# Kernel tuning notes

Measured on AMD Instinct MI355X. Metric: run time of the kernel, lower is better.

The kernel has to match this reference:

```python
import jax, jax.numpy as jnp
import numpy as np

N_EDGE_TYPES = 5  # e_feat compared against 0..4 in message_func


def setup_inputs() -> dict:
    key = jax.random.key(0)
    k1, k2, k3, k4, k5 = jax.random.split(key, 5)
    N, D, E = 50000, 128, 800000
    graph_embedding = jax.random.normal(k1, (N, D), dtype=jnp.float32)
    # xavier_uniform for a (1, D) tensor: bound = sqrt(6 / (1 + D))
    bound = float(np.sqrt(6.0 / (1 + D)))
    weight = jax.random.uniform(k2, (1, D), dtype=jnp.float32, minval=-bound, maxval=bound)
    e_feat = jax.random.randint(k3, (E,), 0, N_EDGE_TYPES, dtype=jnp.int64)
    src = jax.random.randint(k4, (E,), 0, N, dtype=jnp.int64)
    dst = jax.random.randint(k5, (E,), 0, N, dtype=jnp.int64)
    return {"graph_embedding": graph_embedding, "weight": weight,
            "e_feat": e_feat, "src": src, "dst": dst}


def reference(graph_embedding, weight, e_feat, src, dst):
    N = graph_embedding.shape[0]
    # emb == ft == ft0 == ... == ft4 in the original module
    emb = jax.nn.elu(graph_embedding * weight)           # [N, D]
    sft = emb[src]                                       # [E, D] gather src features
    # message = ft_src + sum_t where(e == t, ft_src, 0)
    # since ft0..ft4 all alias emb, the masked sum collapses to
    # sft * (1 + [e in {0..4}]) with exactly one mask firing per edge type.
    et = e_feat.reshape(-1, 1).astype(jnp.float32)       # mirrors e_feat.reshape(-1,1).float()
    hit = (et == jnp.arange(N_EDGE_TYPES, dtype=jnp.float32)[None, :]).sum(axis=1)  # [E]
    msg = sft * (1.0 + hit)[:, None]                     # [E, D]
    # scatter-reduce (sum) over destination nodes == dgl fn.sum('m','ft')
    res = jax.ops.segment_sum(msg, dst, num_segments=N)  # [N, D]
    return res
```

## Files before the change

kernel.cpp:

```cpp
#include <hip/hip_runtime.h>
#include <hip/hip_fp16.h>
#include <math.h>

#define DFEAT 128
#define RSH 6
#define RSZ 64
#define NT  512
#define EPB 4096
#define EPQ (EPB / NT)
#define CHUNK 2048
#define MAXNR 1024
#define TILESH 9
#define TILE (1 << TILESH)
typedef unsigned long long u64;
typedef unsigned int u32;
typedef unsigned short u16;
#define ENDK 0xFFFFFFFFFFFFFFFFULL

__device__ __forceinline__ void elu_store(const float* x, const float* w,
                                          __half* emb2, int i) {
    float4 xv = ((const float4*)x)[i];
    float4 wv = ((const float4*)w)[i & (DFEAT / 4 - 1)];
    float a, r0, r1, r2, r3;
    a = xv.x * wv.x; r0 = 2.0f * (a > 0.0f ? a : (__expf(a) - 1.0f));
    a = xv.y * wv.y; r1 = 2.0f * (a > 0.0f ? a : (__expf(a) - 1.0f));
    a = xv.z * wv.z; r2 = 2.0f * (a > 0.0f ? a : (__expf(a) - 1.0f));
    a = xv.w * wv.w; r3 = 2.0f * (a > 0.0f ? a : (__expf(a) - 1.0f));
    __half2 h01 = __floats2half2_rn(r0, r1);
    __half2 h23 = __floats2half2_rn(r2, r3);
    uint2 pk;
    pk.x = *(u32*)&h01;
    pk.y = *(u32*)&h23;
    ((uint2*)emb2)[i] = pk;
}

__device__ __forceinline__ void scan_tsum_lds(const u32* tsum, u32* ts, int nT) {
    int tid = threadIdx.x;
    u32 v = (tid < nT) ? tsum[tid] : 0u;
    ts[tid] = v;
    __syncthreads();
    for (int d = 1; d < NT; d <<= 1) {
        u32 o = (tid >= d) ? ts[tid - d] : 0u;
        __syncthreads();
        ts[tid] += o;
        __syncthreads();
    }
    u32 incl = ts[tid];
    __syncthreads();
    ts[tid] = incl - v;
    __syncthreads();
}

__global__ __launch_bounds__(NT) void hist_elu_kernel(
        const float* __restrict__ x, const float* __restrict__ w,
        __half* __restrict__ emb2, int total4,
        const int* __restrict__ dst, int E,
        u32* __restrict__ ghist, int EB, int NR) {
    if ((int)blockIdx.x < EB) {
        __shared__ u32 hist[MAXNR];
        int tid = threadIdx.x;
        for (int i = tid; i < NR; i += NT) hist[i] = 0;
        __syncthreads();
        int base = blockIdx.x * EPB;
        for (int q = 0; q < EPQ; ++q) {
            int e = base + tid + q * NT;
            if (e < E) atomicAdd(&hist[(((u32)dst[e]) >> RSH) & (MAXNR - 1)], 1u);
        }
        __syncthreads();
        for (int r = tid; r < NR; r += NT)
            ghist[(size_t)r * EB + blockIdx.x] = hist[r];
    } else {
        int idx = (blockIdx.x - EB) * NT + threadIdx.x;
        if (idx < total4) elu_store(x, w, emb2, idx);
    }
}

__global__ __launch_bounds__(NT) void scan_tile_kernel(
        u32* __restrict__ g, u32* __restrict__ tsum, int M) {
    __shared__ u32 sc[NT];
    int tid = threadIdx.x;
    int i = (blockIdx.x << TILESH) + tid;
    u32 v = (i < M) ? g[i] : 0u;
    sc[tid] = v;
    __syncthreads();
    for (int d = 1; d < NT; d <<= 1) {
        u32 o = (tid >= d) ? sc[tid - d] : 0u;
        __syncthreads();
        sc[tid] += o;
        __syncthreads();
    }
    if (i < M) g[i] = sc[tid] - v;
    if (tid == NT - 1) tsum[blockIdx.x] = sc[NT - 1];
}

__global__ __launch_bounds__(NT) void scatter_pairs_kernel(
        const int* __restrict__ src, const int* __restrict__ dst, int E,
        const u32* __restrict__ ghist, const u32* __restrict__ tsum,
        int EB, int NR, int nT, u32* __restrict__ pairs) {
    __shared__ u32 ts[NT];
    __shared__ u32 off[MAXNR];
    int tid = threadIdx.x;
    scan_tsum_lds(tsum, ts, nT);
    for (int r = tid; r < NR; r += NT) {
        u32 idx = (u32)r * EB + blockIdx.x;
        off[r] = ghist[idx] + ts[idx >> TILESH];
    }
    __syncthreads();
    int base = blockIdx.x * EPB;
    for (int q = 0; q < EPQ; ++q) {
        int e = base + tid + q * NT;
        if (e < E) {
            u32 d = (u32)dst[e];
            u32 s = (u32)src[e];
            u32 p = atomicAdd(&off[(d >> RSH) & (MAXNR - 1)], 1u);
            if (p < (u32)E) pairs[p] = ((d & (RSZ - 1)) << 16) | s;
        }
    }
}

__global__ __launch_bounds__(NT) void gather_sort_kernel(
        const __half* __restrict__ emb2, const u32* __restrict__ pairs,
        const u32* __restrict__ ghist, const u32* __restrict__ tsum,
        int EB, int NR, int nT, int E,
        float* __restrict__ out, int N) {
    __shared__ u32 ts[NT];
    __shared__ u16 sorted[CHUNK];
    __shared__ u32 bcnt[RSZ + 1];
    __shared__ u32 bstart[RSZ + 1];
    int tid = threadIdx.x;
    scan_tsum_lds(tsum, ts, nT);
    int r = blockIdx.x;
    u32 ia = (u32)r * (u32)EB;
    u32 s0 = ghist[ia] + ts[ia >> TILESH];
    u32 s1 = (r + 1 < NR) ? (ghist[ia + EB] + ts[(ia + EB) >> TILESH]) : (u32)E;
    if (s0 > (u32)E) s0 = (u32)E;
    if (s1 > (u32)E) s1 = (u32)E;
    if (s1 < s0) s1 = s0;
    __syncthreads();
    const int wv = tid >> 6;
    const int lane = tid & 63;
    u32 pos = s0;
    do {
        int csz = 0;
        if (s1 > pos) {
            u32 rem = s1 - pos;
            csz = rem < (u32)CHUNK ? (int)rem : CHUNK;
        }
        if (tid < RSZ + 1) bcnt[tid] = 0;
        __syncthreads();
        u32 p0 = 0, p1 = 0, p2 = 0, p3 = 0;
        int  r0 = -1, r1 = -1, r2 = -1, r3 = -1;
        {
            int e0 = tid, e1 = tid + NT, e2 = tid + 2 * NT, e3 = tid + 3 * NT;
            if (e0 < csz) { p0 = pairs[pos + e0]; r0 = (int)(p0 >> 16); }
            if (e1 < csz) { p1 = pairs[pos + e1]; r1 = (int)(p1 >> 16); }
            if (e2 < csz) { p2 = pairs[pos + e2]; r2 = (int)(p2 >> 16); }
            if (e3 < csz) { p3 = pairs[pos + e3]; r3 = (int)(p3 >> 16); }
            if (r0 >= 0) atomicAdd(&bcnt[r0 & (RSZ - 1)], 1u);
            if (r1 >= 0) atomicAdd(&bcnt[r1 & (RSZ - 1)], 1u);
            if (r2 >= 0) atomicAdd(&bcnt[r2 & (RSZ - 1)], 1u);
            if (r3 >= 0) atomicAdd(&bcnt[r3 & (RSZ - 1)], 1u);
        }
        __syncthreads();
        if (tid < RSZ) {
            u32 vv = bcnt[tid];
            u32 inc = vv;
            for (int d = 1; d < RSZ; d <<= 1) {
                u32 o = __shfl_up(inc, d);
                if (lane >= d) inc += o;
            }
            bstart[tid] = inc - vv;
            bcnt[tid]   = inc - vv;
            if (tid == RSZ - 1) bstart[RSZ] = inc;
        }
        __syncthreads();
        if (r0 >= 0) { u32 p = atomicAdd(&bcnt[r0 & (RSZ - 1)], 1u); sorted[p & (CHUNK - 1)] = (u16)(p0 & 0xFFFFu); }
        if (r1 >= 0) { u32 p = atomicAdd(&bcnt[r1 & (RSZ - 1)], 1u); sorted[p & (CHUNK - 1)] = (u16)(p1 & 0xFFFFu); }
        if (r2 >= 0) { u32 p = atomicAdd(&bcnt[r2 & (RSZ - 1)], 1u); sorted[p & (CHUNK - 1)] = (u16)(p2 & 0xFFFFu); }
        if (r3 >= 0) { u32 p = atomicAdd(&bcnt[r3 & (RSZ - 1)], 1u); sorted[p & (CHUNK - 1)] = (u16)(p3 & 0xFFFFu); }
        __syncthreads();
        for (int rr = 0; rr < 8; ++rr) {
            int row = (wv << 3) + rr;
            int n = (r << RSH) + row;
            int jb = (int)bstart[row], je = (int)bstart[row + 1];
            float ax, ay;
            if (pos != s0 && n < N) {
                float2 t = ((const float2*)out)[(size_t)n * (DFEAT / 2) + lane];
                ax = t.x; ay = t.y;
            } else {
                ax = 0.0f; ay = 0.0f;
            }
            for (int j = jb; j < je; j += 8) {
                int last = je - 1;
                int j1 = j + 1 < last ? j + 1 : last;
                int j2 = j + 2 < last ? j + 2 : last;
                int j3 = j + 3 < last ? j + 3 : last;
                int j4 = j + 4 < last ? j + 4 : last;
                int j5 = j + 5 < last ? j + 5 : last;
                int j6 = j + 6 < last ? j + 6 : last;
                int j7 = j + 7 < last ? j + 7 : last;
                u32 q0 = (u32)sorted[j];
                u32 q1 = (u32)sorted[j1];
                u32 q2 = (u32)sorted[j2];
                u32 q3 = (u32)sorted[j3];
                u32 q4 = (u32)sorted[j4];
                u32 q5 = (u32)sorted[j5];
                u32 q6 = (u32)sorted[j6];
                u32 q7 = (u32)sorted[j7];
                u32 h0 = ((const u32*)(emb2 + (size_t)q0 * DFEAT))[lane];
                u32 h1 = ((const u32*)(emb2 + (size_t)q1 * DFEAT))[lane];
                u32 h2 = ((const u32*)(emb2 + (size_t)q2 * DFEAT))[lane];
                u32 h3 = ((const u32*)(emb2 + (size_t)q3 * DFEAT))[lane];
                u32 h4 = ((const u32*)(emb2 + (size_t)q4 * DFEAT))[lane];
                u32 h5 = ((const u32*)(emb2 + (size_t)q5 * DFEAT))[lane];
                u32 h6 = ((const u32*)(emb2 + (size_t)q6 * DFEAT))[lane];
                u32 h7 = ((const u32*)(emb2 + (size_t)q7 * DFEAT))[lane];
                float2 f0 = __half22float2(*(__half2*)&h0);
                ax += f0.x; ay += f0.y;
                if (j + 1 < je) { float2 f = __half22float2(*(__half2*)&h1); ax += f.x; ay += f.y; }
                if (j + 2 < je) { float2 f = __half22float2(*(__half2*)&h2); ax += f.x; ay += f.y; }
                if (j + 3 < je) { float2 f = __half22float2(*(__half2*)&h3); ax += f.x; ay += f.y; }
                if (j + 4 < je) { float2 f = __half22float2(*(__half2*)&h4); ax += f.x; ay += f.y; }
                if (j + 5 < je) { float2 f = __half22float2(*(__half2*)&h5); ax += f.x; ay += f.y; }
                if (j + 6 < je) { float2 f = __half22float2(*(__half2*)&h6); ax += f.x; ay += f.y; }
                if (j + 7 < je) { float2 f = __half22float2(*(__half2*)&h7); ax += f.x; ay += f.y; }
            }
            if (n < N)
                ((float2*)out)[(size_t)n * (DFEAT / 2) + lane] = make_float2(ax, ay);
        }
        __syncthreads();
        pos += CHUNK;
    } while (pos < s1);
}


__global__ void bin_elu_ll_kernel(const float* __restrict__ x,
                                  const float* __restrict__ w,
                                  __half* __restrict__ emb2, int total4,
                                  const int* __restrict__ src,
                                  const int* __restrict__ dst, int E,
                                  u64* __restrict__ head,
                                  u64* __restrict__ nxt,
                                  int binBlocks) {
    if ((int)blockIdx.x < binBlocks) {
        int base = blockIdx.x * 1024 + threadIdx.x;
        for (int q = 0; q < 4; ++q) {
            int e = base + q * 256;
            if (e < E) {
                int s = src[e];
                int d = dst[e];
                u64 old = atomicExch(&head[d], ((u64)(u32)s << 32) | (u32)e);
                nxt[e] = old;
            }
        }
    } else {
        int idx = (blockIdx.x - binBlocks) * blockDim.x + threadIdx.x;
        if (idx >= total4) return;
        elu_store(x, w, emb2, idx);
    }
}

__global__ void gather_ll_kernel(const __half* __restrict__ emb2,
                                 const u64* __restrict__ head,
                                 const u64* __restrict__ nxt,
                                 float* __restrict__ out, int N) {
    int wid = (blockIdx.x * blockDim.x + threadIdx.x) >> 6;
    int lane = threadIdx.x & 63;
    int nA = wid * 2;
    int nB = nA + 1;
    if (nA >= N) return;
    bool hasB = (nB < N);
    u64 curA = head[nA];
    u64 curB = hasB ? head[nB] : ENDK;
    float2 accA = make_float2(0.0f, 0.0f);
    float2 accB = make_float2(0.0f, 0.0f);
    while (curA != ENDK || curB != ENDK) {
        bool aA = (curA != ENDK);
        bool aB = (curB != ENDK);
        u64 cA = curA, cB = curB;
        u32 uA = 0, uB = 0;
        if (aA) uA = ((const u32*)(emb2 + ((size_t)(cA >> 32)) * DFEAT))[lane];
        if (aB) uB = ((const u32*)(emb2 + ((size_t)(cB >> 32)) * DFEAT))[lane];
        if (aA) curA = nxt[(u32)cA];
        if (aB) curB = nxt[(u32)cB];
        if (aA) {
            float2 f = __half22float2(*(__half2*)&uA);
            accA.x += f.x; accA.y += f.y;
        }
        if (aB) {
            float2 f = __half22float2(*(__half2*)&uB);
            accB.x += f.x; accB.y += f.y;
        }
    }
    ((float2*)(out + (size_t)nA * DFEAT))[lane] = accA;
    if (hasB) ((float2*)(out + (size_t)nB * DFEAT))[lane] = accB;
}

__global__ void scatter_fused_kernel(const float* __restrict__ x,
                                     const float* __restrict__ w,
                                     const int* __restrict__ src,
                                     const int* __restrict__ dst,
                                     float* __restrict__ out, int E) {
    int t = blockIdx.x * blockDim.x + threadIdx.x;
    int edge = t >> 5;
    int lane = t & 31;
    if (edge >= E) return;
    int s = src[edge];
    int d = dst[edge];
    float4 xv = ((const float4*)(x + (size_t)s * DFEAT))[lane];
    float4 wv = ((const float4*)w)[lane];
    float4 v;
    float a;
    a = xv.x * wv.x; v.x = 2.0f * (a > 0.0f ? a : (__expf(a) - 1.0f));
    a = xv.y * wv.y; v.y = 2.0f * (a > 0.0f ? a : (__expf(a) - 1.0f));
    a = xv.z * wv.z; v.z = 2.0f * (a > 0.0f ? a : (__expf(a) - 1.0f));
    a = xv.w * wv.w; v.w = 2.0f * (a > 0.0f ? a : (__expf(a) - 1.0f));
    float* op = out + (size_t)d * DFEAT + lane * 4;
    unsafeAtomicAdd(op + 0, v.x);
    unsafeAtomicAdd(op + 1, v.y);
    unsafeAtomicAdd(op + 2, v.z);
    unsafeAtomicAdd(op + 3, v.w);
}

extern "C" void kernel_launch(void* const* d_in, const int* in_sizes, int n_in,
                              void* d_out, int out_size, void* d_ws, size_t ws_size,
                              hipStream_t stream) {
    const float* x   = (const float*)d_in[0];
    const float* w   = (const float*)d_in[1];
    const int*   src = (const int*)d_in[3];
    const int*   dst = (const int*)d_in[4];
    float* out = (float*)d_out;

    const int ND = in_sizes[0];
    const int N  = ND / DFEAT;
    const int E  = in_sizes[2];

    const int EB = (E + EPB - 1) / EPB;
    const int NR = (N + RSZ - 1) >> RSH;
    const int M  = NR * EB;
    const int nT = (M + TILE - 1) >> TILESH;

    size_t emb_bytes   = ((size_t)ND * sizeof(__half) + 15) & ~(size_t)15;
    size_t ghist_bytes = ((size_t)M * sizeof(u32) + 15) & ~(size_t)15;
    size_t tsum_bytes  = ((size_t)NT * sizeof(u32) + 15) & ~(size_t)15;
    size_t pairs_bytes = ((size_t)E * sizeof(u32) + 15) & ~(size_t)15;
    size_t total_new = emb_bytes + ghist_bytes + tsum_bytes + pairs_bytes;

    size_t head64_bytes = ((size_t)N * sizeof(u64) + 15) & ~(size_t)15;
    size_t nxt64_bytes  = ((size_t)E * sizeof(u64) + 15) & ~(size_t)15;
    size_t total_old = emb_bytes + head64_bytes + nxt64_bytes;

    int total4 = ND / 4;

    if (ws_size >= total_new && N <= 65536 && NR <= MAXNR && nT <= NT) {
        char* p = (char*)d_ws;
        __half* emb2  = (__half*)p;  p += emb_bytes;
        u32*    ghist = (u32*)p;     p += ghist_bytes;
        u32*    tsum  = (u32*)p;     p += tsum_bytes;
        u32*    pairs = (u32*)p;

        int eluBlocks = (total4 + NT - 1) / NT;
        hist_elu_kernel<<<EB + eluBlocks, NT, 0, stream>>>(
            x, w, emb2, total4, dst, E, ghist, EB, NR);

        scan_tile_kernel<<<nT, NT, 0, stream>>>(ghist, tsum, M);

        scatter_pairs_kernel<<<EB, NT, 0, stream>>>(
            src, dst, E, ghist, tsum, EB, NR, nT, pairs);

        gather_sort_kernel<<<NR, NT, 0, stream>>>(
            emb2, pairs, ghist, tsum, EB, NR, nT, E, out, N);
    } else if (ws_size >= total_old) {
        char* p = (char*)d_ws;
        __half* emb2 = (__half*)p;  p += emb_bytes;
        u64*    head = (u64*)p;     p += head64_bytes;
        u64*    nxt  = (u64*)p;

        hipMemsetAsync(head, 0xFF, (size_t)N * sizeof(u64), stream);

        int eluBlocks256 = (total4 + 255) / 256;
        int binBlocks = (E + 1023) / 1024;
        bin_elu_ll_kernel<<<binBlocks + eluBlocks256, 256, 0, stream>>>(
            x, w, emb2, total4, src, dst, E, head, nxt, binBlocks);

        long long waves = (N + 1) / 2;
        long long thr = waves * 64;
        gather_ll_kernel<<<(int)((thr + 255) / 256), 256, 0, stream>>>(
            emb2, head, nxt, out, N);
    } else {
        hipMemsetAsync(d_out, 0, (size_t)out_size * sizeof(float), stream);
        long long threads = (long long)E * 32;
        scatter_fused_kernel<<<(int)((threads + 255) / 256), 256, 0, stream>>>(x, w, src, dst, out, E);
    }
}
```

Before: 138.9 us.

## Replace global scan with per-block local offsets and segment collection in gather

The global exclusive scan over the block-by-bucket histogram and its separate scan kernel are removed. Each edge block now computes local bucket offsets itself and writes its pairs contiguously within its own 8192-edge region, staged through LDS so the global writes are coalesced. The gather kernel scans per-block segment counts itself and copies each bucket's segments from all edge blocks into an LDS buffer before the local sort. This saves one launch and the global scan, at the cost of serial per-thread segment copies and a larger LDS footprint in the gather.

```diff
diff --git a/kernel.cpp b/kernel.cpp
--- a/kernel.cpp
+++ b/kernel.cpp
@@ -6,12 +6,10 @@
 #define RSH 6
 #define RSZ 64
 #define NT  512
-#define EPB 4096
+#define EPB 8192
 #define EPQ (EPB / NT)
-#define CHUNK 2048
+#define BUF 8192
 #define MAXNR 1024
-#define TILESH 9
-#define TILE (1 << TILESH)
 typedef unsigned long long u64;
 typedef unsigned int u32;
 typedef unsigned short u16;
@@ -34,157 +32,147 @@
     ((uint2*)emb2)[i] = pk;
 }
 
-__device__ __forceinline__ void scan_tsum_lds(const u32* tsum, u32* ts, int nT) {
-    int tid = threadIdx.x;
-    u32 v = (tid < nT) ? tsum[tid] : 0u;
-    ts[tid] = v;
-    __syncthreads();
-    for (int d = 1; d < NT; d <<= 1) {
-        u32 o = (tid >= d) ? ts[tid - d] : 0u;
-        __syncthreads();
-        ts[tid] += o;
-        __syncthreads();
-    }
-    u32 incl = ts[tid];
-    __syncthreads();
-    ts[tid] = incl - v;
-    __syncthreads();
-}
-
 __global__ __launch_bounds__(NT) void hist_elu_kernel(
         const float* __restrict__ x, const float* __restrict__ w,
         __half* __restrict__ emb2, int total4,
         const int* __restrict__ dst, int E,
-        u32* __restrict__ ghist, int EB, int NR) {
+        u32* __restrict__ loff, int EB, int NR) {
     if ((int)blockIdx.x < EB) {
-        __shared__ u32 hist[MAXNR];
+        __shared__ u32 cnt[MAXNR];
+        __shared__ u32 sb[NT];
         int tid = threadIdx.x;
-        for (int i = tid; i < NR; i += NT) hist[i] = 0;
+        for (int i = tid; i < NR; i += NT) cnt[i] = 0;
         __syncthreads();
         int base = blockIdx.x * EPB;
         for (int q = 0; q < EPQ; ++q) {
             int e = base + tid + q * NT;
-            if (e < E) atomicAdd(&hist[(((u32)dst[e]) >> RSH) & (MAXNR - 1)], 1u);
-        }
-        __syncthreads();
-        for (int r = tid; r < NR; r += NT)
-            ghist[(size_t)r * EB + blockIdx.x] = hist[r];
+            if (e < E) atomicAdd(&cnt[(((u32)dst[e]) >> RSH) & (MAXNR - 1)], 1u);
+        }
+        __syncthreads();
+        u32 c0 = (2 * tid     < NR) ? cnt[2 * tid]     : 0u;
+        u32 c1 = (2 * tid + 1 < NR) ? cnt[2 * tid + 1] : 0u;
+        sb[tid] = c0 + c1;
+        __syncthreads();
+        for (int d = 1; d < NT; d <<= 1) {
+            u32 o = (tid >= d) ? sb[tid - d] : 0u;
+            __syncthreads();
+            sb[tid] += o;
+            __syncthreads();
+        }
+        u32 excl = sb[tid] - (c0 + c1);
+        u32* lrow = loff + (size_t)blockIdx.x * (NR + 1);
+        if (2 * tid     < NR) lrow[2 * tid]     = excl;
+        if (2 * tid + 1 < NR) lrow[2 * tid + 1] = excl + c0;
+        if (tid == 0)         lrow[NR]          = sb[NT - 1];
     } else {
         int idx = (blockIdx.x - EB) * NT + threadIdx.x;
         if (idx < total4) elu_store(x, w, emb2, idx);
     }
 }
 
-__global__ __launch_bounds__(NT) void scan_tile_kernel(
-        u32* __restrict__ g, u32* __restrict__ tsum, int M) {
-    __shared__ u32 sc[NT];
-    int tid = threadIdx.x;
-    int i = (blockIdx.x << TILESH) + tid;
-    u32 v = (i < M) ? g[i] : 0u;
-    sc[tid] = v;
-    __syncthreads();
-    for (int d = 1; d < NT; d <<= 1) {
-        u32 o = (tid >= d) ? sc[tid - d] : 0u;
-        __syncthreads();
-        sc[tid] += o;
-        __syncthreads();
-    }
-    if (i < M) g[i] = sc[tid] - v;
-    if (tid == NT - 1) tsum[blockIdx.x] = sc[NT - 1];
-}
-
 __global__ __launch_bounds__(NT) void scatter_pairs_kernel(
         const int* __restrict__ src, const int* __restrict__ dst, int E,
-        const u32* __restrict__ ghist, const u32* __restrict__ tsum,
-        int EB, int NR, int nT, u32* __restrict__ pairs) {
-    __shared__ u32 ts[NT];
+        const u32* __restrict__ loff, int EB, int NR,
+        u32* __restrict__ pairs) {
     __shared__ u32 off[MAXNR];
+    __shared__ u32 stg[EPB];
     int tid = threadIdx.x;
-    scan_tsum_lds(tsum, ts, nT);
-    for (int r = tid; r < NR; r += NT) {
-        u32 idx = (u32)r * EB + blockIdx.x;
-        off[r] = ghist[idx] + ts[idx >> TILESH];
-    }
+    int c = blockIdx.x;
+    const u32* lrow = loff + (size_t)c * (NR + 1);
+    for (int r = tid; r < NR; r += NT) off[r] = lrow[r];
     __syncthreads();
-    int base = blockIdx.x * EPB;
+    int base = c * EPB;
+    int csz = E - base; if (csz > EPB) csz = EPB;
     for (int q = 0; q < EPQ; ++q) {
         int e = base + tid + q * NT;
         if (e < E) {
             u32 d = (u32)dst[e];
             u32 s = (u32)src[e];
             u32 p = atomicAdd(&off[(d >> RSH) & (MAXNR - 1)], 1u);
-            if (p < (u32)E) pairs[p] = ((d & (RSZ - 1)) << 16) | s;
-        }
-    }
-}
-
-__global__ __launch_bounds__(NT) void gather_sort_kernel(
+            stg[p & (EPB - 1)] = ((d & (RSZ - 1)) << 16) | s;
+        }
+    }
+    __syncthreads();
+    for (int i = tid; i < csz; i += NT)
+        pairs[base + i] = stg[i];
+}
+
+__global__ __launch_bounds__(NT) void gather_kernel(
         const __half* __restrict__ emb2, const u32* __restrict__ pairs,
-        const u32* __restrict__ ghist, const u32* __restrict__ tsum,
-        int EB, int NR, int nT, int E,
+        const u32* __restrict__ loff, int EB, int NR, int E,
         float* __restrict__ out, int N) {
-    __shared__ u32 ts[NT];
-    __shared__ u16 sorted[CHUNK];
-    __shared__ u32 bcnt[RSZ + 1];
+    __shared__ u32 collected[BUF];
+    __shared__ u16 sorted[BUF];
+    __shared__ u32 sb[NT];
     __shared__ u32 bstart[RSZ + 1];
+    __shared__ u32 bplace[RSZ];
+    __shared__ u32 sh_ce;
     int tid = threadIdx.x;
-    scan_tsum_lds(tsum, ts, nT);
     int r = blockIdx.x;
-    u32 ia = (u32)r * (u32)EB;
-    u32 s0 = ghist[ia] + ts[ia >> TILESH];
-    u32 s1 = (r + 1 < NR) ? (ghist[ia + EB] + ts[(ia + EB) >> TILESH]) : (u32)E;
-    if (s0 > (u32)E) s0 = (u32)E;
-    if (s1 > (u32)E) s1 = (u32)E;
-    if (s1 < s0) s1 = s0;
-    __syncthreads();
-    const int wv = tid >> 6;
-    const int lane = tid & 63;
-    u32 pos = s0;
-    do {
-        int csz = 0;
-        if (s1 > pos) {
-            u32 rem = s1 - pos;
-            csz = rem < (u32)CHUNK ? (int)rem : CHUNK;
-        }
-        if (tid < RSZ + 1) bcnt[tid] = 0;
-        __syncthreads();
-        u32 p0 = 0, p1 = 0, p2 = 0, p3 = 0;
-        int  r0 = -1, r1 = -1, r2 = -1, r3 = -1;
-        {
-            int e0 = tid, e1 = tid + NT, e2 = tid + 2 * NT, e3 = tid + 3 * NT;
-            if (e0 < csz) { p0 = pairs[pos + e0]; r0 = (int)(p0 >> 16); }
-            if (e1 < csz) { p1 = pairs[pos + e1]; r1 = (int)(p1 >> 16); }
-            if (e2 < csz) { p2 = pairs[pos + e2]; r2 = (int)(p2 >> 16); }
-            if (e3 < csz) { p3 = pairs[pos + e3]; r3 = (int)(p3 >> 16); }
-            if (r0 >= 0) atomicAdd(&bcnt[r0 & (RSZ - 1)], 1u);
-            if (r1 >= 0) atomicAdd(&bcnt[r1 & (RSZ - 1)], 1u);
-            if (r2 >= 0) atomicAdd(&bcnt[r2 & (RSZ - 1)], 1u);
-            if (r3 >= 0) atomicAdd(&bcnt[r3 & (RSZ - 1)], 1u);
-        }
+    const int wv = tid >> 6, lane = tid & 63;
+    u32 segA = 0, segC = 0;
+    if (tid < EB) {
+        const u32* lrow = loff + (size_t)tid * (NR + 1);
+        segA = lrow[r];
+        segC = lrow[r + 1] - segA;
+        if (segC > (u32)EPB) segC = 0;
+    }
+    bool first = true;
+    int cs = 0;
+    while (cs < EB) {
+        u32 mycnt = (tid >= cs && tid < EB) ? segC : 0u;
+        sb[tid] = mycnt;
+        __syncthreads();
+        for (int d = 1; d < NT; d <<= 1) {
+            u32 o = (tid >= d) ? sb[tid - d] : 0u;
+            __syncthreads();
+            sb[tid] += o;
+            __syncthreads();
+        }
+        u32 incl = sb[tid];
+        u32 base = incl - mycnt;
+        if (tid == 0) sh_ce = (u32)(cs + 1);
+        __syncthreads();
+        bool qok = (tid >= cs && tid < EB && incl <= (u32)BUF);
+        if (qok) atomicMax(&sh_ce, (u32)(tid + 1));
+        __syncthreads();
+        int ce = (int)sh_ce;
+        u32 total = (ce > cs) ? sb[ce - 1] : 0u;
+        if (total > (u32)BUF) total = (u32)BUF;
+        if (tid >= cs && tid < ce && segC > 0) {
+            u32 gbase = (u32)tid * (u32)EPB + segA;
+            for (u32 i = 0; i < segC; ++i)
+                collected[(base + i) & (BUF - 1)] = pairs[gbase + i];
+        }
+        if (tid < RSZ + 1) bstart[tid] = 0;
+        __syncthreads();
+        for (u32 i = tid; i < total; i += NT)
+            atomicAdd(&bstart[(collected[i] >> 16) & (RSZ - 1)], 1u);
         __syncthreads();
         if (tid < RSZ) {
-            u32 vv = bcnt[tid];
+            u32 vv = bstart[tid];
             u32 inc = vv;
             for (int d = 1; d < RSZ; d <<= 1) {
                 u32 o = __shfl_up(inc, d);
                 if (lane >= d) inc += o;
             }
             bstart[tid] = inc - vv;
-            bcnt[tid]   = inc - vv;
+            bplace[tid] = inc - vv;
             if (tid == RSZ - 1) bstart[RSZ] = inc;
         }
         __syncthreads();
-        if (r0 >= 0) { u32 p = atomicAdd(&bcnt[r0 & (RSZ - 1)], 1u); sorted[p & (CHUNK - 1)] = (u16)(p0 & 0xFFFFu); }
-        if (r1 >= 0) { u32 p = atomicAdd(&bcnt[r1 & (RSZ - 1)], 1u); sorted[p & (CHUNK - 1)] = (u16)(p1 & 0xFFFFu); }
-        if (r2 >= 0) { u32 p = atomicAdd(&bcnt[r2 & (RSZ - 1)], 1u); sorted[p & (CHUNK - 1)] = (u16)(p2 & 0xFFFFu); }
-        if (r3 >= 0) { u32 p = atomicAdd(&bcnt[r3 & (RSZ - 1)], 1u); sorted[p & (CHUNK - 1)] = (u16)(p3 & 0xFFFFu); }
+        for (u32 i = tid; i < total; i += NT) {
+            u32 pr = collected[i];
+            u32 p = atomicAdd(&bplace[(pr >> 16) & (RSZ - 1)], 1u);
+            sorted[p & (BUF - 1)] = (u16)(pr & 0xFFFFu);
+        }
         __syncthreads();
         for (int rr = 0; rr < 8; ++rr) {
             int row = (wv << 3) + rr;
             int n = (r << RSH) + row;
             int jb = (int)bstart[row], je = (int)bstart[row + 1];
             float ax, ay;
-            if (pos != s0 && n < N) {
+            if (!first && n < N) {
                 float2 t = ((const float2*)out)[(size_t)n * (DFEAT / 2) + lane];
                 ax = t.x; ay = t.y;
             } else {
@@ -229,8 +217,9 @@
                 ((float2*)out)[(size_t)n * (DFEAT / 2) + lane] = make_float2(ax, ay);
         }
         __syncthreads();
-        pos += CHUNK;
-    } while (pos < s1);
+        first = false;
+        cs = ce;
+    }
 }
 
 
@@ -337,14 +326,11 @@
 
     const int EB = (E + EPB - 1) / EPB;
     const int NR = (N + RSZ - 1) >> RSH;
-    const int M  = NR * EB;
-    const int nT = (M + TILE - 1) >> TILESH;
 
     size_t emb_bytes   = ((size_t)ND * sizeof(__half) + 15) & ~(size_t)15;
-    size_t ghist_bytes = ((size_t)M * sizeof(u32) + 15) & ~(size_t)15;
-    size_t tsum_bytes  = ((size_t)NT * sizeof(u32) + 15) & ~(size_t)15;
+    size_t loff_bytes  = ((size_t)EB * (NR + 1) * sizeof(u32) + 15) & ~(size_t)15;
     size_t pairs_bytes = ((size_t)E * sizeof(u32) + 15) & ~(size_t)15;
-    size_t total_new = emb_bytes + ghist_bytes + tsum_bytes + pairs_bytes;
+    size_t total_new = emb_bytes + loff_bytes + pairs_bytes;
 
     size_t head64_bytes = ((size_t)N * sizeof(u64) + 15) & ~(size_t)15;
     size_t nxt64_bytes  = ((size_t)E * sizeof(u64) + 15) & ~(size_t)15;
@@ -352,24 +338,21 @@
 
     int total4 = ND / 4;
 
-    if (ws_size >= total_new && N <= 65536 && NR <= MAXNR && nT <= NT) {
+    if (ws_size >= total_new && N <= 65536 && NR <= MAXNR && EB <= NT) {
         char* p = (char*)d_ws;
         __half* emb2  = (__half*)p;  p += emb_bytes;
-        u32*    ghist = (u32*)p;     p += ghist_bytes;
-        u32*    tsum  = (u32*)p;     p += tsum_bytes;
+        u32*    loff  = (u32*)p;     p += loff_bytes;
         u32*    pairs = (u32*)p;
 
         int eluBlocks = (total4 + NT - 1) / NT;
         hist_elu_kernel<<<EB + eluBlocks, NT, 0, stream>>>(
-            x, w, emb2, total4, dst, E, ghist, EB, NR);
-
-        scan_tile_kernel<<<nT, NT, 0, stream>>>(ghist, tsum, M);
+            x, w, emb2, total4, dst, E, loff, EB, NR);
 
         scatter_pairs_kernel<<<EB, NT, 0, stream>>>(
-            src, dst, E, ghist, tsum, EB, NR, nT, pairs);
-
-        gather_sort_kernel<<<NR, NT, 0, stream>>>(
-            emb2, pairs, ghist, tsum, EB, NR, nT, E, out, N);
+            src, dst, E, loff, EB, NR, pairs);
+
+        gather_kernel<<<NR, NT, 0, stream>>>(
+            emb2, pairs, loff, EB, NR, E, out, N);
     } else if (ws_size >= total_old) {
         char* p = (char*)d_ws;
         __half* emb2 = (__half*)p;  p += emb_bytes;
```

Result: slower. 159.7 us (+15.0%).
